# Kernel tuning notes

Measured on AMD Instinct MI355X. Metric: run time of the kernel, lower is better.

The kernel has to match this reference:

```python
import jax, jax.numpy as jnp
import numpy as np

N, E, F_IN, H, C, Q = 4096, 131072, 512, 64, 16, 6
ALPHA = 1.0
NITER = 2  # torch.svd_lowrank default power iterations


def setup_inputs() -> dict:
    key = jax.random.key(0)
    ks = jax.random.split(key, 12)
    rn = lambda k, s, sc=0.05: jax.random.normal(k, s, dtype=jnp.float32) * sc
    return {
        'x': jax.random.normal(ks[0], (N, F_IN), dtype=jnp.float32),
        'edge_index': jax.random.randint(ks[1], (2, E), 0, N, dtype=jnp.int32),
        'gcn1_w': rn(ks[2], (F_IN, H)), 'gcn1_b': jnp.zeros((H,), jnp.float32),
        'gcn2_w': rn(ks[3], (H, C)), 'gcn2_b': jnp.zeros((C,), jnp.float32),
        'ptd1_w1': rn(ks[4], (F_IN, H)), 'ptd1_b1': jnp.zeros((H,), jnp.float32),
        'ptd1_w2': rn(ks[5], (H, 1)), 'ptd1_b2': jnp.zeros((1,), jnp.float32),
        'ptd2_w1': rn(ks[6], (H, 32)), 'ptd2_b1': jnp.zeros((32,), jnp.float32),
        'ptd2_w2': rn(ks[7], (32, 1)), 'ptd2_b2': jnp.zeros((1,), jnp.float32),
        'omega1': jax.random.normal(ks[8], (N, Q), dtype=jnp.float32),
        'omega2': jax.random.normal(ks[9], (N, Q), dtype=jnp.float32),
    }


def _mlp2(x, w1, b1, w2, b2):
    return jax.nn.relu(x @ w1 + b1) @ w2 + b2


def _edge_gate(x, src, dst, w1, b1, w2, b2):
    # agg = ptd(x_src - x_dst)**2 ; test branch: s = alpha*sigmoid(agg), clipped to [0,1]
    agg = _mlp2(x[src] - x[dst], w1, b1, w2, b2)
    agg = agg * agg
    s = ALPHA * jax.nn.sigmoid(agg)
    return jnp.clip(s.reshape(-1), 0.0, 1.0)


def _gcn_conv(x, src, dst, ew, w, b):
    # PyG GCNConv with edge_weight: add self-loops (weight 1), symmetric norm, aggregate src->dst
    h = x @ w
    si = jnp.arange(N)
    s_full = jnp.concatenate([src, si])
    d_full = jnp.concatenate([dst, si])
    ew_full = jnp.concatenate([ew, jnp.ones((N,), ew.dtype)])
    deg = jax.ops.segment_sum(ew_full, d_full, num_segments=N)
    dis = jnp.where(deg > 0, jax.lax.rsqrt(jnp.maximum(deg, 1e-12)), 0.0)
    norm = dis[s_full] * ew_full * dis[d_full]
    out = jax.ops.segment_sum(norm[:, None] * h[s_full], d_full, num_segments=N)
    return out + b


def _svd_lowrank_V(A, omega):
    # torch.svd_lowrank(A, q=6, niter=2): randomized range finder + small SVD; returns V [N, Q]
    Qb, _ = jnp.linalg.qr(A @ omega)
    for _ in range(NITER):
        Z, _ = jnp.linalg.qr(A.T @ Qb)
        Qb, _ = jnp.linalg.qr(A @ Z)
    B = Qb.T @ A  # [Q, N]
    _, _, Vh = jnp.linalg.svd(B, full_matrices=False)
    return Vh.T  # [N, Q]


def _nuc_loss(aa, V, deflate_matmul):
    loss = jnp.float32(0.0)
    for k in range(Q):  # fixed small Q=6, structurally sequential deflation
        vi = aa @ V[:, k:k + 1]  # [N,1]
        vi = vi / jnp.linalg.norm(vi)
        vmv = (vi.T @ (aa @ vi))[0, 0]
        vv = (vi.T @ vi)[0, 0]
        loss = loss + jnp.sqrt(jnp.abs(vmv / vv))
        if k > 1:
            outer = vi @ vi.T
            aa = aa - (aa @ outer if deflate_matmul else aa * outer)
    return loss


def reference(x, edge_index, gcn1_w, gcn1_b, gcn2_w, gcn2_b,
              ptd1_w1, ptd1_b1, ptd1_w2, ptd1_b2,
              ptd2_w1, ptd2_b1, ptd2_w2, ptd2_b2, omega1, omega2):
    src, dst = edge_index[0], edge_index[1]

    s_1 = _edge_gate(x, src, dst, ptd1_w1, ptd1_b1, ptd1_w2, ptd1_b2)  # [E]
    x1 = jax.nn.relu(_gcn_conv(x, src, dst, s_1, gcn1_w, gcn1_b))  # [N,H], dropout off (eval)

    s_2 = _edge_gate(x1, src, dst, ptd2_w1, ptd2_b1, ptd2_w2, ptd2_b2)  # [E]
    x_out = _gcn_conv(x1, src, dst, s_2, gcn2_w, gcn2_b)  # [N,C]

    # consistency loss: MSE of centered gates against zeros
    consist = jnp.mean((s_1 - jnp.mean(s_1)) ** 2) + jnp.mean((s_2 - jnp.mean(s_2)) ** 2)

    # dense adjacencies (duplicate edges sum, as in to_dense_adj)
    s1d = jnp.zeros((N, N), jnp.float32).at[src, dst].add(s_1) + 1e-6
    s2d = jnp.zeros((N, N), jnp.float32).at[src, dst].add(s_2) + 1e-6
    aa1 = s1d @ s1d.T
    aa2 = s2d @ s2d.T

    V1 = _svd_lowrank_V(s1d, omega1)
    V2 = _svd_lowrank_V(s2d, omega2)
    nuc = _nuc_loss(aa1, V1, deflate_matmul=False) + _nuc_loss(aa2, V2, deflate_matmul=True)

    top2 = jax.lax.top_k(x_out, 2)[0]
    calib = -top2[:, 0] + top2[:, 1]

    return (jax.nn.log_softmax(x_out, axis=1),
            jax.nn.softmax(x_out, axis=1),
            0.01 * consist + 0.01 * nuc,
            s_1, s_2, jnp.mean(calib))
```

## Files before the change

### kernel.cpp

```cpp
#include <hip/hip_runtime.h>
#include <cmath>

constexpr int N = 4096;
constexpr int EDG = 131072;
constexpr float GEPS = 1e-6f;

__device__ __forceinline__ float* blk_sums(float* vals, int cnt) {
  __shared__ float part[4][16];
  __shared__ float tot[16];
  const int lane = threadIdx.x & 63, wv = threadIdx.x >> 6;
  for (int c = 0; c < cnt; ++c) {
    float v = vals[c];
    for (int off = 32; off; off >>= 1) v += __shfl_down(v, off);
    if (lane == 0) part[wv][c] = v;
  }
  __syncthreads();
  if (threadIdx.x == 0)
    for (int c = 0; c < cnt; ++c)
      tot[c] = part[0][c] + part[1][c] + part[2][c] + part[3][c];
  __syncthreads();
  return tot;
}

__global__ void hist_edges(const int* __restrict__ ei, int* __restrict__ cnt) {
  int e = blockIdx.x * 256 + threadIdx.x;
  atomicAdd(&cnt[ei[e]], 1);
  atomicAdd(&cnt[N + ei[EDG + e]], 1);
}

__global__ __launch_bounds__(256) void scan2x(const int* __restrict__ cnt,
                                              int* __restrict__ rowptr,
                                              int* __restrict__ cur) {
  const int b = blockIdx.x;
  const int* c = cnt + b * N;
  int* rp = rowptr + b * (N + 1);
  int* cu = cur + b * N;
  __shared__ int part[256];
  const int t = threadIdx.x;
  int local[16], s = 0;
  const int base = t * 16;
  for (int i = 0; i < 16; ++i) { local[i] = s; s += c[base + i]; }
  part[t] = s;
  __syncthreads();
  if (t == 0) {
    int acc = 0;
    for (int i = 0; i < 256; ++i) { int v = part[i]; part[i] = acc; acc += v; }
  }
  __syncthreads();
  const int off = part[t];
  for (int i = 0; i < 16; ++i) { rp[base + i] = off + local[i]; cu[base + i] = off + local[i]; }
  if (t == 255) rp[N] = off + s;
}

__global__ void scatter_edges(const int* __restrict__ ei, int* __restrict__ cur,
                              int* __restrict__ col_s, int* __restrict__ perm_s,
                              int* __restrict__ col_d, int* __restrict__ perm_d) {
  int e = blockIdx.x * 256 + threadIdx.x;
  int s = ei[e], d = ei[EDG + e];
  int ps = atomicAdd(&cur[s], 1);
  col_s[ps] = d; perm_s[ps] = e;
  int pd = atomicAdd(&cur[N + d], 1);
  col_d[pd] = s; perm_d[pd] = e;
}

__global__ void gatherdis_om(const float* __restrict__ s, const int* __restrict__ perm_s,
                             const int* __restrict__ perm_d, float* __restrict__ ws_,
                             float* __restrict__ wd_, const float* __restrict__ deg,
                             float* __restrict__ dis, const float* __restrict__ om1,
                             const float* __restrict__ om2, float* __restrict__ SC,
                             int omA, int omB) {
  int p = blockIdx.x * 256 + threadIdx.x;
  ws_[p] = s[perm_s[p]];
  wd_[p] = s[perm_d[p]];
  if (p < N) dis[p] = rsqrtf(deg[p] + 1.0f);
  if (om1 && blockIdx.x < 16) {
    int n = p;
    float vals[12];
#pragma unroll
    for (int k = 0; k < 6; ++k) {
      vals[k] = om1[(size_t)n * 6 + k];
      vals[6 + k] = om2[(size_t)n * 6 + k];
    }
    float* tot = blk_sums(vals, 12);
    if (threadIdx.x == 0)
      for (int c = 0; c < 6; ++c) {
        atomicAdd(&SC[omA + c], tot[c]);
        atomicAdd(&SC[omB + c], tot[6 + c]);
      }
  }
}

__global__ __launch_bounds__(256) void gemm512k(const float* __restrict__ A,
                                                const float* __restrict__ W1,
                                                const float* __restrict__ W2,
                                                float* __restrict__ O1,
                                                float* __restrict__ O2) {
  __shared__ float As[16][33];
  __shared__ float Ws[32][128];
  const int t = threadIdx.x;
  const int rt = t >> 4;
  const int ct = t & 15;
  const int r0 = blockIdx.x * 16;
  const int kh = blockIdx.y * 256;
  float acc[8];
#pragma unroll
  for (int j = 0; j < 8; ++j) acc[j] = 0.f;
  for (int kc = 0; kc < 256; kc += 32) {
    const int kb = kh + kc;
    __syncthreads();
    for (int i = t; i < 512; i += 256) {
      int rr = i >> 5, kk = i & 31;
      As[rr][kk] = A[(size_t)(r0 + rr) * 512 + kb + kk];
    }
    for (int i = t; i < 1024; i += 256) {
      int row = i >> 5, c4 = i & 31;
      float4 v;
      if (c4 < 16) v = *(const float4*)&W1[(size_t)(kb + row) * 64 + c4 * 4];
      else         v = *(const float4*)&W2[(size_t)(kb + row) * 64 + (c4 - 16) * 4];
      *(float4*)&Ws[row][c4 * 4] = v;
    }
    __syncthreads();
#pragma unroll
    for (int kk = 0; kk < 32; ++kk) {
      float a = As[rt][kk];
      float4 b0 = *(const float4*)&Ws[kk][ct * 4];
      float4 b1 = *(const float4*)&Ws[kk][64 + ct * 4];
      acc[0] += a * b0.x; acc[1] += a * b0.y;
      acc[2] += a * b0.z; acc[3] += a * b0.w;
      acc[4] += a * b1.x; acc[5] += a * b1.y;
      acc[6] += a * b1.z; acc[7] += a * b1.w;
    }
  }
  const int r = r0 + rt;
#pragma unroll
  for (int j = 0; j < 4; ++j) {
    atomicAdd(&O1[(size_t)r * 64 + ct * 4 + j], acc[j]);
    atomicAdd(&O2[(size_t)r * 64 + ct * 4 + j], acc[4 + j]);
  }
}

__global__ __launch_bounds__(256) void gemm64(const float* __restrict__ A,
                                              const float* __restrict__ W1,
                                              const float* __restrict__ W2,
                                              float* __restrict__ O1,
                                              float* __restrict__ O2) {
  __shared__ float As[32][65];
  __shared__ float Ws[64][48];
  const int t = threadIdx.x;
  const int r = t >> 3;
  const int cg = t & 7;
  const int r0 = blockIdx.x * 32;
  for (int idx = t; idx < 32 * 64; idx += 256)
    As[idx >> 6][idx & 63] = A[(size_t)(r0 + (idx >> 6)) * 64 + (idx & 63)];
  for (int idx = t; idx < 64 * 48; idx += 256) {
    int kk = idx / 48, c = idx % 48;
    Ws[kk][c] = (c < 32) ? W1[kk * 32 + c] : W2[kk * 16 + c - 32];
  }
  __syncthreads();
  float acc[6] = {0.f, 0.f, 0.f, 0.f, 0.f, 0.f};
  for (int k = 0; k < 64; ++k) {
    float a = As[r][k];
#pragma unroll
    for (int j = 0; j < 6; ++j) acc[j] += a * Ws[k][cg + 8 * j];
  }
  int n = r0 + r;
#pragma unroll
  for (int j = 0; j < 6; ++j) {
    int c = cg + 8 * j;
    if (c < 32) O1[(size_t)n * 32 + c] = acc[j];
    else O2[(size_t)n * 16 + c - 32] = acc[j];
  }
}

__global__ void edge_gate1(const float* __restrict__ xw, const int* __restrict__ ei,
                           const float* __restrict__ b1, const float* __restrict__ w2,
                           const float* __restrict__ b2, float* __restrict__ s_out,
                           float* __restrict__ deg, float* __restrict__ SCs) {
  const int lane = threadIdx.x & 63;
  const int wave = threadIdx.x >> 6;
  const int u = lane >> 4;
  const int q = lane & 15;
  const float4 b1q = ((const float4*)b1)[q];
  const float4 w2q = ((const float4*)w2)[q];
  const float b2s = b2[0];
  const float4* xw4 = (const float4*)xw;
  const int base = blockIdx.x * 64 + wave * 16 + u;
  int sx[4], dx[4];
#pragma unroll
  for (int it = 0; it < 4; ++it) {
    sx[it] = ei[base + it * 4];
    dx[it] = ei[EDG + base + it * 4];
  }
  float4 xs[4], xd[4];
#pragma unroll
  for (int it = 0; it < 4; ++it) xs[it] = xw4[(size_t)sx[it] * 16 + q];
#pragma unroll
  for (int it = 0; it < 4; ++it) xd[it] = xw4[(size_t)dx[it] * 16 + q];
  float g[4];
#pragma unroll
  for (int it = 0; it < 4; ++it)
    g[it] = fmaxf(xs[it].x - xd[it].x + b1q.x, 0.f) * w2q.x
          + fmaxf(xs[it].y - xd[it].y + b1q.y, 0.f) * w2q.y
          + fmaxf(xs[it].z - xd[it].z + b1q.z, 0.f) * w2q.z
          + fmaxf(xs[it].w - xd[it].w + b1q.w, 0.f) * w2q.w;
#pragma unroll
  for (int off = 1; off < 16; off <<= 1)
#pragma unroll
    for (int it = 0; it < 4; ++it) g[it] += __shfl_xor(g[it], off);
  float lsum = 0.f, lssq = 0.f;
  if (q == 0) {
#pragma unroll
    for (int it = 0; it < 4; ++it) {
      float agg = g[it] + b2s;
      agg *= agg;
      float sv = 1.f / (1.f + __expf(-agg));
      s_out[base + it * 4] = sv;
      atomicAdd(&deg[dx[it]], sv);
      lsum += sv; lssq += sv * sv;
    }
  }
  lsum += __shfl_down(lsum, 16); lsum += __shfl_down(lsum, 32);
  lssq += __shfl_down(lssq, 16); lssq += __shfl_down(lssq, 32);
  __shared__ float red[8];
  if (lane == 0) { red[wave] = lsum; red[4 + wave] = lssq; }
  __syncthreads();
  if (threadIdx.x == 0) {
    atomicAdd(&SCs[0], red[0] + red[1] + red[2] + red[3]);
    atomicAdd(&SCs[1], red[4] + red[5] + red[6] + red[7]);
  }
}

__global__ void edge_gate2(const float* __restrict__ xw, const int* __restrict__ ei,
                           const float* __restrict__ b1, const float* __restrict__ w2,
                           const float* __restrict__ b2, float* __restrict__ s_out,
                           float* __restrict__ deg, float* __restrict__ SCs) {
  const int lane = threadIdx.x & 63;
  const int wave = threadIdx.x >> 6;
  const int u = lane >> 3;
  const int q = lane & 7;
  const float4 b1q = ((const float4*)b1)[q];
  const float4 w2q = ((const float4*)w2)[q];
  const float b2s = b2[0];
  const float4* xw4 = (const float4*)xw;
  const int base = blockIdx.x * 128 + wave * 32 + u;
  int sx[4], dx[4];
#pragma unroll
  for (int it = 0; it < 4; ++it) {
    sx[it] = ei[base + it * 8];
    dx[it] = ei[EDG + base + it * 8];
  }
  float4 xs[4], xd[4];
#pragma unroll
  for (int it = 0; it < 4; ++it) xs[it] = xw4[(size_t)sx[it] * 8 + q];
#pragma unroll
  for (int it = 0; it < 4; ++it) xd[it] = xw4[(size_t)dx[it] * 8 + q];
  float g[4];
#pragma unroll
  for (int it = 0; it < 4; ++it)
    g[it] = fmaxf(xs[it].x - xd[it].x + b1q.x, 0.f) * w2q.x
          + fmaxf(xs[it].y - xd[it].y + b1q.y, 0.f) * w2q.y
          + fmaxf(xs[it].z - xd[it].z + b1q.z, 0.f) * w2q.z
          + fmaxf(xs[it].w - xd[it].w + b1q.w, 0.f) * w2q.w;
#pragma unroll
  for (int off = 1; off < 8; off <<= 1)
#pragma unroll
    for (int it = 0; it < 4; ++it) g[it] += __shfl_xor(g[it], off);
  float lsum = 0.f, lssq = 0.f;
  if (q == 0) {
#pragma unroll
    for (int it = 0; it < 4; ++it) {
      float agg = g[it] + b2s;
      agg *= agg;
      float sv = 1.f / (1.f + __expf(-agg));
      s_out[base + it * 8] = sv;
      atomicAdd(&deg[dx[it]], sv);
      lsum += sv; lssq += sv * sv;
    }
  }
  lsum += __shfl_down(lsum, 8); lsum += __shfl_down(lsum, 16); lsum += __shfl_down(lsum, 32);
  lssq += __shfl_down(lssq, 8); lssq += __shfl_down(lssq, 16); lssq += __shfl_down(lssq, 32);
  __shared__ float red[8];
  if (lane == 0) { red[wave] = lsum; red[4 + wave] = lssq; }
  __syncthreads();
  if (threadIdx.x == 0) {
    atomicAdd(&SCs[0], red[0] + red[1] + red[2] + red[3]);
    atomicAdd(&SCs[1], red[4] + red[5] + red[6] + red[7]);
  }
}

__global__ void conv1f(const int* __restrict__ rp, const int* __restrict__ cl,
                       const float* __restrict__ w, const float* __restrict__ h1,
                       const float* __restrict__ dis, const float* __restrict__ bias,
                       float* __restrict__ x1) {
  const int lane = threadIdx.x & 63, wv = threadIdx.x >> 6;
  const int es = lane >> 4;
  const int q = lane & 15;
  const int r = blockIdx.x * 4 + wv;
  const int e0 = rp[r], e1 = rp[r + 1];
  const float4* h14 = (const float4*)h1;
  float ax = 0.f, ay = 0.f, az = 0.f, aw = 0.f;
  int e = e0 + es;
  for (; e + 4 < e1; e += 8) {
    int c0 = cl[e], c1 = cl[e + 4];
    float w0 = w[e] * dis[c0], w1_ = w[e + 4] * dis[c1];
    float4 h0 = h14[(size_t)c0 * 16 + q];
    float4 h1v = h14[(size_t)c1 * 16 + q];
    ax += w0 * h0.x + w1_ * h1v.x;
    ay += w0 * h0.y + w1_ * h1v.y;
    az += w0 * h0.z + w1_ * h1v.z;
    aw += w0 * h0.w + w1_ * h1v.w;
  }
  for (; e < e1; e += 4) {
    int c = cl[e];
    float wx = w[e] * dis[c];
    float4 hv = h14[(size_t)c * 16 + q];
    ax += wx * hv.x; ay += wx * hv.y; az += wx * hv.z; aw += wx * hv.w;
  }
  ax += __shfl_xor(ax, 16); ax += __shfl_xor(ax, 32);
  ay += __shfl_xor(ay, 16); ay += __shfl_xor(ay, 32);
  az += __shfl_xor(az, 16); az += __shfl_xor(az, 32);
  aw += __shfl_xor(aw, 16); aw += __shfl_xor(aw, 32);
  if (es == 0) {
    float d = dis[r];
    float4 hh = h14[(size_t)r * 16 + q];
    float4 bq = ((const float4*)bias)[q];
    float4 o;
    o.x = fmaxf(d * (ax + d * hh.x) + bq.x, 0.f);
    o.y = fmaxf(d * (ay + d * hh.y) + bq.y, 0.f);
    o.z = fmaxf(d * (az + d * hh.z) + bq.z, 0.f);
    o.w = fmaxf(d * (aw + d * hh.w) + bq.w, 0.f);
    ((float4*)x1)[(size_t)r * 16 + q] = o;
  }
}

__global__ void conv2f(const int* __restrict__ rp, const int* __restrict__ cl,
                       const float* __restrict__ w, const float* __restrict__ h2,
                       const float* __restrict__ dis, const float* __restrict__ bias,
                       float* __restrict__ xo) {
  const int lane = threadIdx.x & 63, wv = threadIdx.x >> 6;
  const int es = lane >> 2;
  const int q = lane & 3;
  const int r = blockIdx.x * 4 + wv;
  const int e0 = rp[r], e1 = rp[r + 1];
  const float4* h24 = (const float4*)h2;
  float ax = 0.f, ay = 0.f, az = 0.f, aw = 0.f;
  for (int e = e0 + es; e < e1; e += 16) {
    int c = cl[e];
    float wx = w[e] * dis[c];
    float4 hv = h24[(size_t)c * 4 + q];
    ax += wx * hv.x; ay += wx * hv.y; az += wx * hv.z; aw += wx * hv.w;
  }
#pragma unroll
  for (int off = 4; off < 64; off <<= 1) {
    ax += __shfl_xor(ax, off);
    ay += __shfl_xor(ay, off);
    az += __shfl_xor(az, off);
    aw += __shfl_xor(aw, off);
  }
  if (es == 0) {
    float d = dis[r];
    float4 hh = h24[(size_t)r * 4 + q];
    float4 bq = ((const float4*)bias)[q];
    float4 o;
    o.x = d * (ax + d * hh.x) + bq.x;
    o.y = d * (ay + d * hh.y) + bq.y;
    o.z = d * (az + d * hh.z) + bq.z;
    o.w = d * (aw + d * hh.w) + bq.w;
    ((float4*)xo)[(size_t)r * 4 + q] = o;
  }
}

__global__ void softmax_calib(const float* __restrict__ xo, float* __restrict__ ls,
                              float* __restrict__ sm, float* __restrict__ SC) {
  const int t = threadIdx.x;
  const int r = blockIdx.x * 256 + t;
  float v[16];
  float mx = -3.0e38f, mx2 = -3.0e38f;
#pragma unroll
  for (int c = 0; c < 16; ++c) {
    v[c] = xo[(size_t)r * 16 + c];
    if (v[c] > mx) { mx2 = mx; mx = v[c]; }
    else if (v[c] > mx2) mx2 = v[c];
  }
  float se = 0.f;
#pragma unroll
  for (int c = 0; c < 16; ++c) se += expf(v[c] - mx);
  const float lse = mx + logf(se);
#pragma unroll
  for (int c = 0; c < 16; ++c) {
    float z = v[c] - lse;
    ls[(size_t)r * 16 + c] = z;
    sm[(size_t)r * 16 + c] = expf(z);
  }
  float calib = mx2 - mx;
  float* tot = blk_sums(&calib, 1);
  if (t == 0) atomicAdd(&SC[4], tot[0]);
}

template<int NORM, int SX>
__global__ __launch_bounds__(256) void spmm8f(
    const int* __restrict__ rp, const int* __restrict__ cl,
    const float* __restrict__ wA, const float* __restrict__ wB,
    const float* __restrict__ XA, const float* __restrict__ XB,
    float* __restrict__ OA, float* __restrict__ OB,
    const double* __restrict__ GpA, const double* __restrict__ GpB,
    double* __restrict__ GnA, double* __restrict__ GnB,
    float* __restrict__ SC, int cspA, int cspB, int csoA, int csoB) {
  __shared__ float Rinv[2][36];
  __shared__ float csn[2][8];
  __shared__ float bs[2][8];
  __shared__ float gpart[8][21];
  const int t = threadIdx.x;
  if (NORM) {
    if (t < 2) {
      const double* G = t ? GpB : GpA;
      const float* csp = SC + (t ? cspB : cspA);
      float Gf[6][6];
      int p = 0;
      for (int i = 0; i < 6; ++i)
        for (int j = i; j < 6; ++j) { float gv = (float)G[p]; Gf[i][j] = gv; Gf[j][i] = gv; ++p; }
      float Rm[6][6];
      for (int i = 0; i < 6; ++i) for (int j = 0; j < 6; ++j) Rm[i][j] = 0.f;
      for (int j = 0; j < 6; ++j) {
        float s = Gf[j][j];
        for (int k = 0; k < j; ++k) s -= Rm[k][j] * Rm[k][j];
        float dj = sqrtf(fmaxf(s, 1e-30f));
        Rm[j][j] = dj;
        for (int i = j + 1; i < 6; ++i) {
          float v = Gf[j][i];
          for (int k = 0; k < j; ++k) v -= Rm[k][j] * Rm[k][i];
          Rm[j][i] = v / dj;
        }
      }
      float Ri[6][6];
      for (int j = 0; j < 6; ++j) {
        Ri[j][j] = 1.f / Rm[j][j];
        for (int i = j - 1; i >= 0; --i) {
          float s = 0.f;
          for (int k = i + 1; k <= j; ++k) s += Rm[i][k] * Ri[k][j];
          Ri[i][j] = -s / Rm[i][i];
        }
      }
      for (int i = 0; i < 6; ++i)
        for (int j = 0; j < 6; ++j)
          Rinv[t][i * 6 + j] = (j >= i) ? Ri[i][j] : 0.f;
      for (int f = 0; f < 8; ++f) {
        float s = 0.f;
        if (f < 6)
          for (int j = 0; j <= f; ++j) s += csp[j] * Ri[j][f];
        csn[t][f] = s;
      }
    }
  } else {
    if (t < 16) {
      int h = t >> 3, f = t & 7;
      csn[h][f] = (f < 6) ? SC[(h ? cspB : cspA) + f] : 0.f;
    }
  }
  if (t < 16) bs[t >> 3][t & 7] = 0.f;
  __syncthreads();
  const int lane = t & 63, wv = t >> 6;
  const int half = lane >> 5, la = lane & 31;
  const int f = la & 7, es = la >> 3;
  const float* w = half ? wB : wA;
  const float* X = half ? XB : XA;
  float* O = half ? OB : OA;
  const float* Ri = Rinv[half];
  const float epsf = csn[half][f] * GEPS;
  float gp[6];
#pragma unroll
  for (int j = 0; j < 6; ++j) gp[j] = 0.f;
  for (int rr = 0; rr < 2; ++rr) {
    const int r = blockIdx.x * 8 + wv * 2 + rr;
    const int e0 = rp[r], e1 = rp[r + 1];
    float acc = 0.f;
    if (f < 6) {
      for (int e = e0 + es; e < e1; e += 4) {
        int c = cl[e];
        const float* xr = X + (size_t)c * SX;
        float xn;
        if (NORM) {
          xn = 0.f;
          for (int j = 0; j <= f; ++j) xn += xr[j] * Ri[j * 6 + f];
        } else {
          xn = xr[f];
        }
        acc += w[e] * xn;
      }
    }
    acc += __shfl_xor(acc, 8);
    acc += __shfl_xor(acc, 16);
    float o = acc + epsf;
    float ov[6];
#pragma unroll
    for (int j = 0; j < 6; ++j) ov[j] = __shfl(o, half * 32 + j);
    if (es == 0) {
      O[((size_t)r << 3) + f] = o;
      if (f < 6) {
        atomicAdd(&bs[half][f], o);
#pragma unroll
        for (int j = 0; j < 6; ++j)
          if (j >= f) gp[j - f] += o * ov[j];
      }
    }
  }
  if (es == 0 && f < 6) {
    int p0 = f * 6 - (f * (f - 1)) / 2;
    for (int j = 0; j < 6 - f; ++j) gpart[wv * 2 + half][p0 + j] = gp[j];
  }
  __syncthreads();
  if (t < 42) {
    int h = t / 21, p = t % 21;
    float s = gpart[h][p] + gpart[2 + h][p] + gpart[4 + h][p] + gpart[6 + h][p];
    atomicAdd(&(h ? GnB : GnA)[p], (double)s);
  }
  if (t < 16) {
    int h = t >> 3, ff = t & 7;
    if (ff < 6) atomicAdd(&SC[(h ? csoB : csoA) + ff], bs[h][ff]);
  }
}

template<int F, int DIS>
__global__ __launch_bounds__(256) void spmm(const int* __restrict__ rowptr,
                                            const int* __restrict__ col,
                                            const float* __restrict__ w,
                                            const float* __restrict__ X,
                                            const float* __restrict__ dis,
                                            float* __restrict__ OUT,
                                            float* __restrict__ SC, int cs_idx,
                                            float eps, int osum, int ossq) {
  constexpr int ES = 64 / F;
  const int lane = threadIdx.x & 63;
  const int wv = threadIdx.x >> 6;
  const int f = lane & (F - 1);
  const int es = lane / F;
  const int r = blockIdx.x * 4 + wv;
  const int e0 = rowptr[r], e1 = rowptr[r + 1];
  float acc = 0.f;
  for (int e = e0 + es; e < e1; e += ES) {
    int c = col[e];
    float wx = w[e];
    if (DIS) wx *= dis[c];
    acc += wx * X[(size_t)c * F + f];
  }
#pragma unroll
  for (int off = F; off < 64; off <<= 1) acc += __shfl_xor(acc, off);
  float o = acc + ((cs_idx >= 0) ? eps * SC[cs_idx + f] : 0.f);
  if (es == 0) OUT[(size_t)r * F + f] = o;
  if (osum >= 0 || ossq >= 0) {
    __shared__ float bs[8], bq[8];
    if (threadIdx.x < F) { bs[threadIdx.x] = 0.f; bq[threadIdx.x] = 0.f; }
    __syncthreads();
    if (es == 0) {
      if (osum >= 0) atomicAdd(&bs[f], o);
      if (ossq >= 0) atomicAdd(&bq[f], o * o);
    }
    __syncthreads();
    if (threadIdx.x < F) {
      if (osum >= 0) atomicAdd(&SC[osum + threadIdx.x], bs[threadIdx.x]);
      if (ossq >= 0) atomicAdd(&SC[ossq + threadIdx.x], bq[threadIdx.x]);
    }
  }
}

template<int FA, int FB>
__global__ __launch_bounds__(256) void spmm2(const int* __restrict__ rowptr,
                                             const int* __restrict__ col,
                                             const float* __restrict__ wA,
                                             const float* __restrict__ wB,
                                             const float* __restrict__ XA,
                                             const float* __restrict__ XB,
                                             float* __restrict__ OA,
                                             float* __restrict__ OB,
                                             float* __restrict__ SC,
                                             int csA, int csB, float eps,
                                             int osumA, int ossqA, int osumB, int ossqB) {
  const int lane = threadIdx.x & 63;
  const int wv = threadIdx.x >> 6;
  const int half = lane >> 5;
  const int la = lane & 31;
  const int F = half ? FB : FA;
  const int f = la & (F - 1);
  const int es = la / F;
  const int ES = 32 / F;
  const int r = blockIdx.x * 4 + wv;
  const int e0 = rowptr[r], e1 = rowptr[r + 1];
  const float* w = half ? wB : wA;
  const float* X = half ? XB : XA;
  float acc = 0.f;
// ... 106 lines not shown
  __shared__ float WsA[36], rsA[6], WsB[36], rsB[6];
  if (threadIdx.x < 36) { WsA[threadIdx.x] = SMFA[threadIdx.x]; WsB[threadIdx.x] = SMFB[threadIdx.x]; }
  if (threadIdx.x < 6) { rsA[threadIdx.x] = SMFA[36 + threadIdx.x]; rsB[threadIdx.x] = SMFB[36 + threadIdx.x]; }
  __syncthreads();
  int n = blockIdx.x * 256 + threadIdx.x;
  float ba[6], bb[6];
#pragma unroll
  for (int j = 0; j < 6; ++j) { ba[j] = BtA[(size_t)n * 8 + j]; bb[j] = BtB[(size_t)n * 8 + j]; }
  float vals[6];
#pragma unroll
  for (int k = 0; k < 6; ++k) {
    float sa = 0.f, sb = 0.f;
#pragma unroll
    for (int j = 0; j < 6; ++j) { sa += ba[j] * WsA[j * 6 + k]; sb += bb[j] * WsB[j * 6 + k]; }
    sa *= rsA[k]; sb *= rsB[k];
    V8A[(size_t)n * 8 + k] = sa;
    V8B[(size_t)n * 8 + k] = sb;
    if (k < 3) {
      WA[(size_t)n * 4 + k] = sa;
      WB[(size_t)n * 4 + k] = sb;
      vals[k] = sa; vals[3 + k] = sb;
    }
  }
  V8A[(size_t)n * 8 + 6] = 0.f; V8A[(size_t)n * 8 + 7] = 0.f;
  V8B[(size_t)n * 8 + 6] = 0.f; V8B[(size_t)n * 8 + 7] = 0.f;
  WA[(size_t)n * 4 + 3] = 0.f;
  WB[(size_t)n * 4 + 3] = 0.f;
  float* tot = blk_sums(vals, 6);
  if (threadIdx.x == 0)
    for (int c = 0; c < 3; ++c) {
      atomicAdd(&SC[sA + c], tot[c]);
      atomicAdd(&SC[sB + c], tot[3 + c]);
    }
}

__global__ void b3post(const float* __restrict__ YA, const float* __restrict__ YB,
                       const float* __restrict__ ZZB, float* __restrict__ UvA,
                       float* __restrict__ UvB, float* __restrict__ WB,
                       float* __restrict__ SC, int zzA, int nyA, int zzB, int nyB,
                       int sWp) {
  if (blockIdx.x == 0 && threadIdx.x == 0) {
    float add = 0.f;
    for (int k = 0; k < 3; ++k) add += sqrtf(fabsf(SC[zzA + k] / SC[nyA + k]));
    for (int k = 0; k < 3; ++k) add += sqrtf(fabsf(SC[zzB + k] / SC[nyB + k]));
    SC[5] += add;
  }
  int n = blockIdx.x * 256 + threadIdx.x;
  UvA[n] = YA[(size_t)n * 4 + 2] * rsqrtf(SC[nyA + 2]);
  UvB[n] = YB[(size_t)n * 4 + 2] * rsqrtf(SC[nyB + 2]);
  float v = ZZB[(size_t)n * 4 + 2] * rsqrtf(SC[nyB + 2]);
  WB[(size_t)n * 4 + 0] = v;
  WB[(size_t)n * 4 + 1] = 0.f;
  WB[(size_t)n * 4 + 2] = 0.f;
  WB[(size_t)n * 4 + 3] = 0.f;
  float* tot = blk_sums(&v, 1);
  if (threadIdx.x == 0) atomicAdd(&SC[sWp], tot[0]);
}

__global__ void buildAB(float* __restrict__ WA, int FCpad, int nt, int nu,
                        const float* __restrict__ V8A, int kcol,
                        const float* __restrict__ UvA, float* __restrict__ SC, int sWa,
                        float* __restrict__ WB, const float* __restrict__ V8B,
                        const float* __restrict__ UvB, int nd, int sWb, int Cidx,
                        const float* __restrict__ P4, float* __restrict__ Pv,
                        int pvmode, int prevdp, int prevny) {
  const int bid = blockIdx.x;
  const int n = (bid & 15) * 256 + threadIdx.x;
  if (bid < 16) {
    float bv = V8A[(size_t)n * 8 + kcol];
    float uv[3];
    for (int b = 0; b < 3; ++b) uv[b] = (b < nu) ? UvA[(size_t)b * N + n] : 0.f;
    float vals[8];
    for (int t = 0; t < FCpad; ++t) {
      float v = 0.f;
      if (t < nt) {
        v = bv;
        for (int b = 0; b < nu; ++b)
          if ((t >> b) & 1) v *= uv[b];
      }
      WA[(size_t)n * FCpad + t] = v;
      vals[t] = v;
    }
    float* tot = blk_sums(vals, nt);
    if (threadIdx.x == 0)
      for (int c = 0; c < nt; ++c) atomicAdd(&SC[sWa + c], tot[c]);
  } else {
    if (pvmode == 1) {
      Pv[n] = P4[(size_t)n * 4];
    } else if (pvmode >= 2) {
      float crs = rsqrtf(SC[prevny]);
      float s = P4[(size_t)n * 4];
      s -= SC[prevdp + 1] * crs * Pv[n];
      if (pvmode == 3) s -= SC[prevdp + 3] * crs * Pv[(size_t)N + n];
      Pv[(size_t)(pvmode - 1) * N + n] = s;
    }
    float v = V8B[(size_t)n * 8 + kcol];
    WB[(size_t)n * 4 + 0] = v;
    WB[(size_t)n * 4 + 1] = 0.f;
    WB[(size_t)n * 4 + 2] = 0.f;
    WB[(size_t)n * 4 + 3] = 0.f;
    float vals[4];
    vals[0] = v;
    for (int t = 0; t < 3; ++t) vals[1 + t] = (t < nd) ? UvB[(size_t)t * N + n] * v : 0.f;
    float* tot = blk_sums(vals, 1 + nd);
    if (threadIdx.x == 0) {
      atomicAdd(&SC[sWb], tot[0]);
      for (int t = 0; t < nd; ++t) atomicAdd(&SC[Cidx + t], tot[1 + t]);
    }
  }
}

__global__ void epibuild(const float* __restrict__ YA, int FA, int nt, int nu,
                         const float* __restrict__ UvA, float* __restrict__ yvA, int nyA2,
                         float* __restrict__ WA, int sW2a,
                         const float* __restrict__ YB, const float* __restrict__ Pv,
                         const float* __restrict__ UvB, int nd, float* __restrict__ yvB,
                         int Cidx, int nyB2, int dp, float* __restrict__ WB, int sW2b,
                         float* __restrict__ SC) {
  const int bid = blockIdx.x;
  const int n = (bid & 15) * 256 + threadIdx.x;
  if (bid < 16) {
    float uv[3];
    for (int b = 0; b < 3; ++b) uv[b] = (b < nu) ? UvA[(size_t)b * N + n] : 0.f;
    float s = 0.f;
    for (int t = 0; t < nt; ++t) {
      float w = YA[(size_t)n * FA + t];
      int pc = 0;
      for (int b = 0; b < nu; ++b)
        if ((t >> b) & 1) { w *= uv[b]; ++pc; }
      s += (pc & 1) ? -w : w;
    }
    yvA[n] = s;
    float v = s * s;
    float* tot = blk_sums(&v, 1);
    if (threadIdx.x == 0) atomicAdd(&SC[nyA2], tot[0]);
    float vals[8];
    for (int t = 0; t < FA; ++t) {
      float v2 = 0.f;
      if (t < nt) {
        v2 = s;
        for (int b = 0; b < nu; ++b)
          if ((t >> b) & 1) v2 *= uv[b];
      }
      WA[(size_t)n * FA + t] = v2;
      vals[t] = v2;
    }
    float* tot2 = blk_sums(vals, nt);
    if (threadIdx.x == 0)
      for (int c = 0; c < nt; ++c) atomicAdd(&SC[sW2a + c], tot2[c]);
  } else {
    float y = YB[(size_t)n * 4];
    for (int t = 0; t < nd; ++t) y -= SC[Cidx + t] * Pv[(size_t)t * N + n];
    yvB[n] = y;
    float vals[7];
    vals[0] = y * y;
    for (int t = 0; t < 3; ++t) {
      vals[1 + 2 * t] = (t < nd) ? y * Pv[(size_t)t * N + n] : 0.f;
      vals[2 + 2 * t] = (t < nd) ? UvB[(size_t)t * N + n] * y : 0.f;
    }
    float* tot = blk_sums(vals, 1 + 2 * nd);
    if (threadIdx.x == 0) {
      atomicAdd(&SC[nyB2], tot[0]);
      for (int i = 0; i < 2 * nd; ++i) atomicAdd(&SC[dp + i], tot[1 + i]);
    }
    WB[(size_t)n * 4 + 0] = y;
    WB[(size_t)n * 4 + 1] = 0.f;
    WB[(size_t)n * 4 + 2] = 0.f;
    WB[(size_t)n * 4 + 3] = 0.f;
    float yy = y;
    float* tot2 = blk_sums(&yy, 1);
    if (threadIdx.x == 0) atomicAdd(&SC[sW2b], tot2[0]);
  }
}

__global__ void defpost(float* __restrict__ SC, int zzA2, int nt, int nyA2,
                        int zzB2, int nyB2, int dp, int nd,
                        const float* __restrict__ yvA, const float* __restrict__ yvB,
                        float* __restrict__ UvA, float* __restrict__ UvB, int k,
                        const float* __restrict__ ZZB, float* __restrict__ WB,
                        int sW3, int dobuild, int dofin, float* __restrict__ outp) {
  if (blockIdx.x == 0 && threadIdx.x == 0) {
    float vmv = 0.f;
    for (int t = 0; t < nt; ++t) {
      int pc = __popc(t);
      vmv += (pc & 1) ? -SC[zzA2 + t] : SC[zzA2 + t];
    }
    float add = sqrtf(fabsf(vmv / SC[nyA2]));
    float vb = SC[zzB2];
    for (int t = 0; t < nd; ++t) vb -= SC[dp + 2 * t] * SC[dp + 2 * t + 1];
    add += sqrtf(fabsf(vb / SC[nyB2]));
    SC[5] += add;
    if (dofin) {
      const float Ef = (float)EDG;
      float m1 = SC[0] / Ef, v1 = SC[1] / Ef - m1 * m1;
      float m2 = SC[2] / Ef, v2 = SC[3] / Ef - m2 * m2;
      outp[131072] = 0.01f * (v1 + v2) + 0.01f * SC[5];
      outp[393217] = SC[4] / (float)N;
    }
  }
  if (dobuild) {
    int n = blockIdx.x * 256 + threadIdx.x;
    UvA[(size_t)(k - 2) * N + n] = yvA[n] * rsqrtf(SC[nyA2]);
    UvB[(size_t)(k - 2) * N + n] = yvB[n] * rsqrtf(SC[nyB2]);
    float v = ZZB[(size_t)n * 4 + 0] * rsqrtf(SC[nyB2]);
    WB[(size_t)n * 4 + 0] = v;
    WB[(size_t)n * 4 + 1] = 0.f;
    WB[(size_t)n * 4 + 2] = 0.f;
    WB[(size_t)n * 4 + 3] = 0.f;
    float* tot = blk_sums(&v, 1);
    if (threadIdx.x == 0) atomicAdd(&SC[sW3], tot[0]);
  }
}

extern "C" void kernel_launch(void* const* d_in, const int* in_sizes, int n_in,
                              void* d_out, int out_size, void* d_ws, size_t ws_size,
                              hipStream_t stream) {
  const float* x      = (const float*)d_in[0];
  const int*   ei     = (const int*)  d_in[1];
  const float* gcn1_w = (const float*)d_in[2];
  const float* gcn1_b = (const float*)d_in[3];
  const float* gcn2_w = (const float*)d_in[4];
  const float* gcn2_b = (const float*)d_in[5];
  const float* p1w1   = (const float*)d_in[6];
  const float* p1b1   = (const float*)d_in[7];
  const float* p1w2   = (const float*)d_in[8];
  const float* p1b2   = (const float*)d_in[9];
  const float* p2w1   = (const float*)d_in[10];
  const float* p2b1   = (const float*)d_in[11];
  const float* p2w2   = (const float*)d_in[12];
  const float* p2b2   = (const float*)d_in[13];
  const float* omega1 = (const float*)d_in[14];
  const float* omega2 = (const float*)d_in[15];
  float* out = (float*)d_out;

  float* ws = (float*)d_ws;
  size_t o = 0;
  auto alloc = [&](size_t nf) { float* p = ws + o; o += nf; return p; };
  float* xw1  = alloc((size_t)N * 64);
  float* h1   = alloc((size_t)N * 64);
  double* Gd  = (double*)(ws + o); o += 576;
  int* cnt    = (int*)(ws + o);    o += 2 * N;
  float* deg1 = alloc(N);
  float* deg2 = alloc(N);
  float* SC   = alloc(1024);
  const size_t zero_bytes = o * sizeof(float);
  float* x1   = alloc((size_t)N * 64);
  float* x1w  = alloc((size_t)N * 32);
  float* h2   = alloc((size_t)N * 16);
  float* xo   = alloc((size_t)N * 16);
  float* dis1 = alloc(N);
  float* dis2 = alloc(N);
  float* QA   = alloc((size_t)N * 8);
  float* QB   = alloc((size_t)N * 8);
  float* ZA   = alloc((size_t)N * 8);
  float* ZB   = alloc((size_t)N * 8);
  float* BtA  = alloc((size_t)N * 8);
  float* BtB  = alloc((size_t)N * 8);
  float* V8A  = alloc((size_t)N * 8);
  float* V8B  = alloc((size_t)N * 8);
  float* WA   = alloc((size_t)N * 8);
  float* WB   = alloc((size_t)N * 4);
  float* TA   = alloc((size_t)N * 8);
  float* TB   = alloc((size_t)N * 4);
  float* YA   = alloc((size_t)N * 8);
  float* YB   = alloc((size_t)N * 4);
  float* ZZA  = alloc((size_t)N * 8);
  float* ZZB  = alloc((size_t)N * 4);
  float* P4   = alloc((size_t)N * 4);
  float* yvA  = alloc(N);
  float* yvB  = alloc(N);
  float* UvA  = alloc((size_t)3 * N);
  float* UvB  = alloc((size_t)3 * N);
  float* Pv   = alloc((size_t)3 * N);
  float* SMFA = alloc(64);
  float* SMFB = alloc(64);
  int* rowptr = (int*)alloc(2 * (N + 1) + 2);
  int* cur    = (int*)alloc(2 * N);
  int* col_s  = (int*)alloc(EDG);
  int* perm_s = (int*)alloc(EDG);
  int* col_d  = (int*)alloc(EDG);
  int* perm_d = (int*)alloc(EDG);
  float* w1s  = alloc(EDG);
  float* w1d  = alloc(EDG);
  float* w2s  = alloc(EDG);
  float* w2d  = alloc(EDG);
  if (ws_size < o * sizeof(float)) return;

  const int* rp_s = rowptr;
  const int* rp_d = rowptr + (N + 1);

  int cs = 8;
  auto NS = [&]() { int s = cs; cs += 8; return s; };
  int gslot = 0;
  auto NG = [&]() { int g = gslot; gslot += 24; return g; };

  hipMemsetAsync(ws, 0, zero_bytes, stream);
  hist_edges<<<512, 256, 0, stream>>>(ei, cnt);
  scan2x<<<2, 256, 0, stream>>>(cnt, rowptr, cur);
  scatter_edges<<<512, 256, 0, stream>>>(ei, cur, col_s, perm_s, col_d, perm_d);

  int omA = NS(), omB = NS();

  gemm512k<<<dim3(256, 2), 256, 0, stream>>>(x, p1w1, gcn1_w, xw1, h1);
  edge_gate1<<<2048, 256, 0, stream>>>(xw1, ei, p1b1, p1w2, p1b2,
                                       out + 131073, deg1, SC);
  gatherdis_om<<<512, 256, 0, stream>>>(out + 131073, perm_s, perm_d, w1s, w1d,
                                        deg1, dis1, omega1, omega2, SC, omA, omB);
  conv1f<<<1024, 256, 0, stream>>>(rp_d, col_d, w1d, h1, dis1, gcn1_b, x1);

  gemm64<<<128, 256, 0, stream>>>(x1, p2w1, gcn2_w, x1w, h2);
  edge_gate2<<<1024, 256, 0, stream>>>(x1w, ei, p2b1, p2w2, p2b2,
                                       out + 262145, deg2, SC + 2);
  gatherdis_om<<<512, 256, 0, stream>>>(out + 262145, perm_s, perm_d, w2s, w2d,
                                        deg2, dis2, nullptr, nullptr, SC, 0, 0);
  conv2f<<<1024, 256, 0, stream>>>(rp_d, col_d, w2d, h2, dis2, gcn2_b, xo);
  softmax_calib<<<16, 256, 0, stream>>>(xo, out, out + 65536, SC);

  int g0a = NG(), g0b = NG(), g1a = NG(), g1b = NG(), g2a = NG(), g2b = NG();
  int g3a = NG(), g3b = NG(), g4a = NG(), g4b = NG(), g5a = NG(), g5b = NG();
  int c0a = NS(), c0b = NS(), c1a = NS(), c1b = NS(), c2a = NS(), c2b = NS();
  int c3a = NS(), c3b = NS(), c4a = NS(), c4b = NS(), c5a = NS(), c5b = NS();
  spmm8f<0, 6><<<512, 256, 0, stream>>>(rp_s, col_s, w1s, w2s, omega1, omega2,
                                        QA, QB, nullptr, nullptr, Gd + g0a, Gd + g0b,
                                        SC, omA, omB, c0a, c0b);
  spmm8f<1, 8><<<512, 256, 0, stream>>>(rp_d, col_d, w1d, w2d, QA, QB, ZA, ZB,
                                        Gd + g0a, Gd + g0b, Gd + g1a, Gd + g1b,
                                        SC, c0a, c0b, c1a, c1b);
  spmm8f<1, 8><<<512, 256, 0, stream>>>(rp_s, col_s, w1s, w2s, ZA, ZB, QA, QB,
                                        Gd + g1a, Gd + g1b, Gd + g2a, Gd + g2b,
                                        SC, c1a, c1b, c2a, c2b);
  spmm8f<1, 8><<<512, 256, 0, stream>>>(rp_d, col_d, w1d, w2d, QA, QB, ZA, ZB,
                                        Gd + g2a, Gd + g2b, Gd + g3a, Gd + g3b,
                                        SC, c2a, c2b, c3a, c3b);
  spmm8f<1, 8><<<512, 256, 0, stream>>>(rp_s, col_s, w1s, w2s, ZA, ZB, QA, QB,
                                        Gd + g3a, Gd + g3b, Gd + g4a, Gd + g4b,
                                        SC, c3a, c3b, c4a, c4b);
  spmm8f<1, 8><<<512, 256, 0, stream>>>(rp_d, col_d, w1d, w2d, QA, QB, BtA, BtB,
                                        Gd + g4a, Gd + g4b, Gd + g5a, Gd + g5b,
                                        SC, c4a, c4b, c5a, c5b);
  jacobi2<<<1, 128, 0, stream>>>(Gd + g5a, Gd + g5b, SMFA, SMFB);

  int sWa = NS(), sWb = NS();
  v_scale_pack<<<16, 256, 0, stream>>>(BtA, SMFA, BtB, SMFB, V8A, V8B, WA, WB,
                                       SC, sWa, sWb);
  int sTa = NS(), sTb = NS();
  spmm2<4, 4><<<1024, 256, 0, stream>>>(rp_d, col_d, w1d, w2d, WA, WB, TA, TB,
                                        SC, sWa, sWb, GEPS, sTa, -1, sTb, -1);
  int sYa = NS(), sYb = NS(), nyA = NS(), nyB = NS();
  spmm2<4, 4><<<1024, 256, 0, stream>>>(rp_s, col_s, w1s, w2s, TA, TB, YA, YB,
                                        SC, sTa, sTb, GEPS, sYa, nyA, sYb, nyB);
  int zzA = NS(), zzB = NS();
  spmm2<4, 4><<<1024, 256, 0, stream>>>(rp_d, col_d, w1d, w2d, YA, YB, ZZA, ZZB,
                                        SC, sYa, sYb, GEPS, -1, zzA, -1, zzB);
  int sWp = NS();
  b3post<<<16, 256, 0, stream>>>(YA, YB, ZZB, UvA, UvB, WB, SC, zzA, nyA, zzB, nyB, sWp);
  spmm<4, 0><<<1024, 256, 0, stream>>>(rp_s, col_s, w2s, WB, nullptr, P4, SC, sWp,
                                       GEPS, -1, -1);

  int dp_prev = 0, ny_prev = 0;
  for (int k = 3; k <= 5; ++k) {
    const int nu = k - 2, nt = 1 << nu, nd = k - 2;
    const int FA = (k < 5) ? 4 : 8;
    int dWa = NS(), dWb = NS(), C = NS();
    int dTa = NS(), dTb = NS();
    int nyA2 = NS(), nyB2 = NS(), sW2a = NS(), sW2b = NS(), zzA2 = NS(), zzB2 = NS();
    int dp = NS(), sW3 = NS();
    const int pvmode = (k == 3) ? 1 : (k == 4 ? 2 : 3);
    buildAB<<<32, 256, 0, stream>>>(WA, FA, nt, nu, V8A, k, UvA, SC, dWa,
                                    WB, V8B, UvB, nd, dWb, C, P4, Pv,
                                    pvmode, dp_prev, ny_prev);
    if (FA == 4) {
      spmm2<4, 4><<<1024, 256, 0, stream>>>(rp_d, col_d, w1d, w2d, WA, WB, TA, TB,
                                            SC, dWa, dWb, GEPS, dTa, -1, dTb, -1);
      spmm2<4, 4><<<1024, 256, 0, stream>>>(rp_s, col_s, w1s, w2s, TA, TB, YA, YB,
                                            SC, dTa, dTb, GEPS, -1, -1, -1, -1);
    } else {
      spmm2<8, 4><<<1024, 256, 0, stream>>>(rp_d, col_d, w1d, w2d, WA, WB, TA, TB,
                                            SC, dWa, dWb, GEPS, dTa, -1, dTb, -1);
      spmm2<8, 4><<<1024, 256, 0, stream>>>(rp_s, col_s, w1s, w2s, TA, TB, YA, YB,
                                            SC, dTa, dTb, GEPS, -1, -1, -1, -1);
    }
    epibuild<<<32, 256, 0, stream>>>(YA, FA, nt, nu, UvA, yvA, nyA2, WA, sW2a,
                                     YB, Pv, UvB, nd, yvB, C, nyB2, dp, WB, sW2b, SC);
    if (FA == 4)
      spmm2<4, 4><<<1024, 256, 0, stream>>>(rp_d, col_d, w1d, w2d, WA, WB, ZZA, ZZB,
                                            SC, sW2a, sW2b, GEPS, -1, zzA2, -1, zzB2);
    else
      spmm2<8, 4><<<1024, 256, 0, stream>>>(rp_d, col_d, w1d, w2d, WA, WB, ZZA, ZZB,
                                            SC, sW2a, sW2b, GEPS, -1, zzA2, -1, zzB2);
    if (k < 5) {
      defpost<<<16, 256, 0, stream>>>(SC, zzA2, nt, nyA2, zzB2, nyB2, dp, nd,
                                      yvA, yvB, UvA, UvB, k, ZZB, WB, sW3, 1, 0, out);
      spmm<4, 0><<<1024, 256, 0, stream>>>(rp_s, col_s, w2s, WB, nullptr, P4, SC, sW3,
                                           GEPS, -1, -1);
    } else {
      defpost<<<1, 256, 0, stream>>>(SC, zzA2, nt, nyA2, zzB2, nyB2, dp, nd,
                                     yvA, yvB, UvA, UvB, k, ZZB, WB, sW3, 0, 1, out);
    }
    dp_prev = dp; ny_prev = nyB2;
  }
}
```

Baseline: 788.5 us.

## Compute edge gates in source-CSR order and write sorted gate weights directly

The edge-gate kernels now walk the source-sorted CSR, one wave per source node. Each wave loads the source row's features once and gathers only the destination rows. Gate values are written both to the output (through perm) and directly into the source-ordered weight array, so the gather pass no longer builds the source-ordered copy. This trades coalesced edge-order stores for scattered output writes and adds per-row load imbalance in exchange for fewer feature gathers and one less gather pass.

```diff
diff --git a/kernel.cpp b/kernel.cpp
--- a/kernel.cpp
+++ b/kernel.cpp
@@ -63,14 +63,13 @@
   col_d[pd] = s; perm_d[pd] = e;
 }
 
-__global__ void gatherdis_om(const float* __restrict__ s, const int* __restrict__ perm_s,
-                             const int* __restrict__ perm_d, float* __restrict__ ws_,
+__global__ void gatherdis_om(const float* __restrict__ s,
+                             const int* __restrict__ perm_d,
                              float* __restrict__ wd_, const float* __restrict__ deg,
                              float* __restrict__ dis, const float* __restrict__ om1,
                              const float* __restrict__ om2, float* __restrict__ SC,
                              int omA, int omB) {
   int p = blockIdx.x * 256 + threadIdx.x;
-  ws_[p] = s[perm_s[p]];
   wd_[p] = s[perm_d[p]];
   if (p < N) dis[p] = rsqrtf(deg[p] + 1.0f);
   if (om1 && blockIdx.x < 16) {
@@ -172,10 +171,12 @@
   }
 }
 
-__global__ void edge_gate1(const float* __restrict__ xw, const int* __restrict__ ei,
-                           const float* __restrict__ b1, const float* __restrict__ w2,
-                           const float* __restrict__ b2, float* __restrict__ s_out,
-                           float* __restrict__ deg, float* __restrict__ SCs) {
+__global__ void edge_gate1c(const float* __restrict__ xw, const int* __restrict__ rp,
+                            const int* __restrict__ cl, const int* __restrict__ perm,
+                            const float* __restrict__ b1, const float* __restrict__ w2,
+                            const float* __restrict__ b2, float* __restrict__ s_out,
+                            float* __restrict__ wcs, float* __restrict__ deg,
+                            float* __restrict__ SCs) {
   const int lane = threadIdx.x & 63;
   const int wave = threadIdx.x >> 6;
   const int u = lane >> 4;
@@ -184,56 +185,71 @@
   const float4 w2q = ((const float4*)w2)[q];
   const float b2s = b2[0];
   const float4* xw4 = (const float4*)xw;
-  const int base = blockIdx.x * 64 + wave * 16 + u;
-  int sx[4], dx[4];
-#pragma unroll
-  for (int it = 0; it < 4; ++it) {
-    sx[it] = ei[base + it * 4];
-    dx[it] = ei[EDG + base + it * 4];
-  }
-  float4 xs[4], xd[4];
-#pragma unroll
-  for (int it = 0; it < 4; ++it) xs[it] = xw4[(size_t)sx[it] * 16 + q];
-#pragma unroll
-  for (int it = 0; it < 4; ++it) xd[it] = xw4[(size_t)dx[it] * 16 + q];
-  float g[4];
-#pragma unroll
-  for (int it = 0; it < 4; ++it)
-    g[it] = fmaxf(xs[it].x - xd[it].x + b1q.x, 0.f) * w2q.x
-          + fmaxf(xs[it].y - xd[it].y + b1q.y, 0.f) * w2q.y
-          + fmaxf(xs[it].z - xd[it].z + b1q.z, 0.f) * w2q.z
-          + fmaxf(xs[it].w - xd[it].w + b1q.w, 0.f) * w2q.w;
-#pragma unroll
-  for (int off = 1; off < 16; off <<= 1)
-#pragma unroll
-    for (int it = 0; it < 4; ++it) g[it] += __shfl_xor(g[it], off);
+  const int r = blockIdx.x * 4 + wave;
+  const float4 xsr = xw4[(size_t)r * 16 + q];
+  const int e0 = rp[r], e1 = rp[r + 1];
   float lsum = 0.f, lssq = 0.f;
-  if (q == 0) {
-#pragma unroll
-    for (int it = 0; it < 4; ++it) {
-      float agg = g[it] + b2s;
-      agg *= agg;
-      float sv = 1.f / (1.f + __expf(-agg));
-      s_out[base + it * 4] = sv;
-      atomicAdd(&deg[dx[it]], sv);
+  int e = e0 + u;
+  for (; e + 4 < e1; e += 8) {
+    int d0 = cl[e], d1 = cl[e + 4];
+    float4 xd0 = xw4[(size_t)d0 * 16 + q];
+    float4 xd1 = xw4[(size_t)d1 * 16 + q];
+    float g0 = fmaxf(xsr.x - xd0.x + b1q.x, 0.f) * w2q.x
+             + fmaxf(xsr.y - xd0.y + b1q.y, 0.f) * w2q.y
+             + fmaxf(xsr.z - xd0.z + b1q.z, 0.f) * w2q.z
+             + fmaxf(xsr.w - xd0.w + b1q.w, 0.f) * w2q.w;
+    float g1 = fmaxf(xsr.x - xd1.x + b1q.x, 0.f) * w2q.x
+             + fmaxf(xsr.y - xd1.y + b1q.y, 0.f) * w2q.y
+             + fmaxf(xsr.z - xd1.z + b1q.z, 0.f) * w2q.z
+             + fmaxf(xsr.w - xd1.w + b1q.w, 0.f) * w2q.w;
+#pragma unroll
+    for (int off = 1; off < 16; off <<= 1) {
+      g0 += __shfl_xor(g0, off);
+      g1 += __shfl_xor(g1, off);
+    }
+    if (q == 0) {
+      float a0 = g0 + b2s; a0 *= a0;
+      float a1 = g1 + b2s; a1 *= a1;
+      float s0 = 1.f / (1.f + __expf(-a0));
+      float s1 = 1.f / (1.f + __expf(-a1));
+      s_out[perm[e]] = s0;     wcs[e] = s0;
+      s_out[perm[e + 4]] = s1; wcs[e + 4] = s1;
+      atomicAdd(&deg[d0], s0);
+      atomicAdd(&deg[d1], s1);
+      lsum += s0 + s1; lssq += s0 * s0 + s1 * s1;
+    }
+  }
+  for (; e < e1; e += 4) {
+    int d = cl[e];
+    float4 xd = xw4[(size_t)d * 16 + q];
+    float g = fmaxf(xsr.x - xd.x + b1q.x, 0.f) * w2q.x
+            + fmaxf(xsr.y - xd.y + b1q.y, 0.f) * w2q.y
+            + fmaxf(xsr.z - xd.z + b1q.z, 0.f) * w2q.z
+            + fmaxf(xsr.w - xd.w + b1q.w, 0.f) * w2q.w;
+#pragma unroll
+    for (int off = 1; off < 16; off <<= 1) g += __shfl_xor(g, off);
+    if (q == 0) {
+      float a = g + b2s; a *= a;
+      float sv = 1.f / (1.f + __expf(-a));
+      s_out[perm[e]] = sv; wcs[e] = sv;
+      atomicAdd(&deg[d], sv);
       lsum += sv; lssq += sv * sv;
     }
   }
-  lsum += __shfl_down(lsum, 16); lsum += __shfl_down(lsum, 32);
-  lssq += __shfl_down(lssq, 16); lssq += __shfl_down(lssq, 32);
-  __shared__ float red[8];
-  if (lane == 0) { red[wave] = lsum; red[4 + wave] = lssq; }
-  __syncthreads();
+  float* tot = blk_sums(&lsum, 1);
+  float* tot2 = blk_sums(&lssq, 1);
   if (threadIdx.x == 0) {
-    atomicAdd(&SCs[0], red[0] + red[1] + red[2] + red[3]);
-    atomicAdd(&SCs[1], red[4] + red[5] + red[6] + red[7]);
-  }
-}
-
-__global__ void edge_gate2(const float* __restrict__ xw, const int* __restrict__ ei,
-                           const float* __restrict__ b1, const float* __restrict__ w2,
-                           const float* __restrict__ b2, float* __restrict__ s_out,
-                           float* __restrict__ deg, float* __restrict__ SCs) {
+    atomicAdd(&SCs[0], tot[0]);
+    atomicAdd(&SCs[1], tot2[0]);
+  }
+}
+
+__global__ void edge_gate2c(const float* __restrict__ xw, const int* __restrict__ rp,
+                            const int* __restrict__ cl, const int* __restrict__ perm,
+                            const float* __restrict__ b1, const float* __restrict__ w2,
+                            const float* __restrict__ b2, float* __restrict__ s_out,
+                            float* __restrict__ wcs, float* __restrict__ deg,
+                            float* __restrict__ SCs) {
   const int lane = threadIdx.x & 63;
   const int wave = threadIdx.x >> 6;
   const int u = lane >> 3;
@@ -242,49 +258,62 @@
   const float4 w2q = ((const float4*)w2)[q];
   const float b2s = b2[0];
   const float4* xw4 = (const float4*)xw;
-  const int base = blockIdx.x * 128 + wave * 32 + u;
-  int sx[4], dx[4];
-#pragma unroll
-  for (int it = 0; it < 4; ++it) {
-    sx[it] = ei[base + it * 8];
-    dx[it] = ei[EDG + base + it * 8];
-  }
-  float4 xs[4], xd[4];
-#pragma unroll
-  for (int it = 0; it < 4; ++it) xs[it] = xw4[(size_t)sx[it] * 8 + q];
-#pragma unroll
-  for (int it = 0; it < 4; ++it) xd[it] = xw4[(size_t)dx[it] * 8 + q];
-  float g[4];
-#pragma unroll
-  for (int it = 0; it < 4; ++it)
-    g[it] = fmaxf(xs[it].x - xd[it].x + b1q.x, 0.f) * w2q.x
-          + fmaxf(xs[it].y - xd[it].y + b1q.y, 0.f) * w2q.y
-          + fmaxf(xs[it].z - xd[it].z + b1q.z, 0.f) * w2q.z
-          + fmaxf(xs[it].w - xd[it].w + b1q.w, 0.f) * w2q.w;
-#pragma unroll
-  for (int off = 1; off < 8; off <<= 1)
-#pragma unroll
-    for (int it = 0; it < 4; ++it) g[it] += __shfl_xor(g[it], off);
+  const int r = blockIdx.x * 4 + wave;
+  const float4 xsr = xw4[(size_t)r * 8 + q];
+  const int e0 = rp[r], e1 = rp[r + 1];
   float lsum = 0.f, lssq = 0.f;
-  if (q == 0) {
-#pragma unroll
-    for (int it = 0; it < 4; ++it) {
-      float agg = g[it] + b2s;
-      agg *= agg;
-      float sv = 1.f / (1.f + __expf(-agg));
-      s_out[base + it * 8] = sv;
-      atomicAdd(&deg[dx[it]], sv);
+  int e = e0 + u;
+  for (; e + 8 < e1; e += 16) {
+    int d0 = cl[e], d1 = cl[e + 8];
+    float4 xd0 = xw4[(size_t)d0 * 8 + q];
+    float4 xd1 = xw4[(size_t)d1 * 8 + q];
+    float g0 = fmaxf(xsr.x - xd0.x + b1q.x, 0.f) * w2q.x
+             + fmaxf(xsr.y - xd0.y + b1q.y, 0.f) * w2q.y
+             + fmaxf(xsr.z - xd0.z + b1q.z, 0.f) * w2q.z
+             + fmaxf(xsr.w - xd0.w + b1q.w, 0.f) * w2q.w;
+    float g1 = fmaxf(xsr.x - xd1.x + b1q.x, 0.f) * w2q.x
+             + fmaxf(xsr.y - xd1.y + b1q.y, 0.f) * w2q.y
+             + fmaxf(xsr.z - xd1.z + b1q.z, 0.f) * w2q.z
+             + fmaxf(xsr.w - xd1.w + b1q.w, 0.f) * w2q.w;
+#pragma unroll
+    for (int off = 1; off < 8; off <<= 1) {
+      g0 += __shfl_xor(g0, off);
+      g1 += __shfl_xor(g1, off);
+    }
+    if (q == 0) {
+      float a0 = g0 + b2s; a0 *= a0;
+      float a1 = g1 + b2s; a1 *= a1;
+      float s0 = 1.f / (1.f + __expf(-a0));
+      float s1 = 1.f / (1.f + __expf(-a1));
+      s_out[perm[e]] = s0;     wcs[e] = s0;
+      s_out[perm[e + 8]] = s1; wcs[e + 8] = s1;
+      atomicAdd(&deg[d0], s0);
+      atomicAdd(&deg[d1], s1);
+      lsum += s0 + s1; lssq += s0 * s0 + s1 * s1;
+    }
+  }
+  for (; e < e1; e += 8) {
+    int d = cl[e];
+    float4 xd = xw4[(size_t)d * 8 + q];
+    float g = fmaxf(xsr.x - xd.x + b1q.x, 0.f) * w2q.x
+            + fmaxf(xsr.y - xd.y + b1q.y, 0.f) * w2q.y
+            + fmaxf(xsr.z - xd.z + b1q.z, 0.f) * w2q.z
+            + fmaxf(xsr.w - xd.w + b1q.w, 0.f) * w2q.w;
+#pragma unroll
+    for (int off = 1; off < 8; off <<= 1) g += __shfl_xor(g, off);
+    if (q == 0) {
+      float a = g + b2s; a *= a;
+      float sv = 1.f / (1.f + __expf(-a));
+      s_out[perm[e]] = sv; wcs[e] = sv;
+      atomicAdd(&deg[d], sv);
       lsum += sv; lssq += sv * sv;
     }
   }
-  lsum += __shfl_down(lsum, 8); lsum += __shfl_down(lsum, 16); lsum += __shfl_down(lsum, 32);
-  lssq += __shfl_down(lssq, 8); lssq += __shfl_down(lssq, 16); lssq += __shfl_down(lssq, 32);
-  __shared__ float red[8];
-  if (lane == 0) { red[wave] = lsum; red[4 + wave] = lssq; }
-  __syncthreads();
+  float* tot = blk_sums(&lsum, 1);
+  float* tot2 = blk_sums(&lssq, 1);
   if (threadIdx.x == 0) {
-    atomicAdd(&SCs[0], red[0] + red[1] + red[2] + red[3]);
-    atomicAdd(&SCs[1], red[4] + red[5] + red[6] + red[7]);
+    atomicAdd(&SCs[2], tot[0]);
+    atomicAdd(&SCs[3], tot2[0]);
   }
 }
 
@@ -997,16 +1026,16 @@
   int omA = NS(), omB = NS();
 
   gemm512k<<<dim3(256, 2), 256, 0, stream>>>(x, p1w1, gcn1_w, xw1, h1);
-  edge_gate1<<<2048, 256, 0, stream>>>(xw1, ei, p1b1, p1w2, p1b2,
-                                       out + 131073, deg1, SC);
-  gatherdis_om<<<512, 256, 0, stream>>>(out + 131073, perm_s, perm_d, w1s, w1d,
+  edge_gate1c<<<1024, 256, 0, stream>>>(xw1, rp_s, col_s, perm_s, p1b1, p1w2, p1b2,
+                                        out + 131073, w1s, deg1, SC);
+  gatherdis_om<<<512, 256, 0, stream>>>(out + 131073, perm_d, w1d,
                                         deg1, dis1, omega1, omega2, SC, omA, omB);
   conv1f<<<1024, 256, 0, stream>>>(rp_d, col_d, w1d, h1, dis1, gcn1_b, x1);
 
   gemm64<<<128, 256, 0, stream>>>(x1, p2w1, gcn2_w, x1w, h2);
-  edge_gate2<<<1024, 256, 0, stream>>>(x1w, ei, p2b1, p2w2, p2b2,
-                                       out + 262145, deg2, SC + 2);
-  gatherdis_om<<<512, 256, 0, stream>>>(out + 262145, perm_s, perm_d, w2s, w2d,
+  edge_gate2c<<<1024, 256, 0, stream>>>(x1w, rp_s, col_s, perm_s, p2b1, p2w2, p2b2,
+                                        out + 262145, w2s, deg2, SC);
+  gatherdis_om<<<512, 256, 0, stream>>>(out + 262145, perm_d, w2d,
                                         deg2, dis2, nullptr, nullptr, SC, 0, 0);
   conv2f<<<1024, 256, 0, stream>>>(rp_d, col_d, w2d, h2, dis2, gcn2_b, xo);
   softmax_calib<<<16, 256, 0, stream>>>(xo, out, out + 65536, SC);
```

After: 781.8 us. About the same (-0.8%).
